# Kernel optimization log

Measured on AMD Instinct MI355X. Metric: run time of the kernel, lower is better.

## Reference

```python
import jax, jax.numpy as jnp
import numpy as np

BINS = 10
VMIN = 0.0
VMAX = 1.0
SIGMA = 150.0
DELTA = (VMAX - VMIN) / BINS


def setup_inputs() -> dict:
    key = jax.random.key(0)
    kx, ky = jax.random.split(key)
    x = jax.random.uniform(kx, (16, 3, 512, 512), dtype=jnp.float32)
    y = jax.random.uniform(ky, (16, 3, 512, 512), dtype=jnp.float32)
    return {"x": x, "y": y}


def _soft_hist(img):
    # img: [B, 3, H, W] -> soft histogram [B, 3, BINS]
    centers = VMIN + DELTA * (jnp.arange(BINS, dtype=img.dtype) + 0.5)
    d = img[..., None] - centers  # [B, 3, H, W, BINS]
    w = jax.nn.sigmoid(SIGMA * (d + DELTA / 2)) - jax.nn.sigmoid(SIGMA * (d - DELTA / 2))
    return w.sum(axis=(2, 3))  # sum over all pixels


def reference(x, y):
    B = x.shape[0]
    hx = _soft_hist(x)  # [B, 3, BINS]
    hy = _soft_hist(y)
    # L1Loss (mean over bins) per (batch, channel), summed over batch and channels
    running = jnp.abs(hx - hy).mean(axis=-1).sum()
    return (running / B) * 0.0001
```

## Files before the change

### kernel.cpp

```cpp
#include <hip/hip_runtime.h>


static constexpr int PLANES   = 48;
static constexpr int PLANE_PX = 512 * 512;
static constexpr int SPP      = 32;
static constexpr int THREADS  = 256;
static constexpr int CHUNK    = PLANE_PX / SPP;
static constexpr int NBLK     = 96 * SPP;
static constexpr float E15    = 3269017.3724721107f;

__global__ __launch_bounds__(THREADS, 8) void soft_hist_partial(
    const float* __restrict__ xin, const float* __restrict__ yin,
    unsigned* __restrict__ G )
{
  __shared__ unsigned hist[10 * THREADS];
  __shared__ unsigned red[10 * 16 * 3];
  const int t = threadIdx.x;
  #pragma unroll
  for (int s = 0; s < 10; ++s) hist[s * THREADS + t] = 0u;
  __syncthreads();

  const int blk   = blockIdx.x;
  const int plane = blk >> 5;
  const int sub   = blk & 31;
  const float* src = (plane < PLANES ? xin + (size_t)plane * PLANE_PX
                                     : yin + (size_t)(plane - PLANES) * PLANE_PX)
                   + (size_t)sub * CHUNK;
  const float4* src4 = (const float4*)src;
  unsigned* mycol = hist + t;

  constexpr int ITERS = CHUNK / (THREADS * 4);
  #pragma unroll
  for (int it = 0; it < ITERS; ++it) {
    float4 v4 = src4[it * THREADS + t];
    float vv[4] = {v4.x, v4.y, v4.z, v4.w};
    #pragma unroll
    for (int j = 0; j < 4; ++j) {
      float wv = vv[j] * 10.0f;
      float kf = fminf(floorf(wv), 9.0f);
      int   k  = (int)kf;
      float d  = wv - kf;
      float ex = __expf(d * -15.0f);
      float t1 = 1.0f + ex;
      float t2 = fmaf(E15, ex, 1.0f);
      float r  = __builtin_amdgcn_rcpf(t1 * t2);
      unsigned qa = (unsigned)fmaf(r * t2, 512.0f, 0.5f);
      unsigned qb = (unsigned)fmaf(r * t1, 64.0f, 0.5f);
      atomicAdd(&mycol[k << 8], (qa << 17) + (qb << 6) + 1u);
    }
  }
  __syncthreads();

  if (t < 160) {
    const int bin = t >> 4, grp = t & 15;
    const uint4* hp = (const uint4*)(hist + (bin << 8) + (grp << 4));
    unsigned sa = 0, sb = 0, sc = 0;
    #pragma unroll
    for (int q = 0; q < 4; ++q) {
      uint4 u4 = hp[q];
      unsigned uu[4] = {u4.x, u4.y, u4.z, u4.w};
      #pragma unroll
      for (int e = 0; e < 4; ++e) {
        unsigned u = uu[e];
        sa += u >> 17; sb += (u >> 6) & 0x7FFu; sc += u & 0x3Fu;
      }
    }
    const int base = (bin * 16 + grp) * 3;
    red[base] = sa; red[base + 1] = sb; red[base + 2] = sc;
  }
  __syncthreads();

  if (t < 30) {
    const int bin = t / 3, c = t - 3 * bin;
    unsigned s = 0;
    #pragma unroll
    for (int g = 0; g < 16; ++g) s += red[(bin * 16 + g) * 3 + c];
    G[blk * 32 + bin * 3 + c] = s;
  }
}

__global__ __launch_bounds__(1024) void soft_hist_loss(
    const unsigned* __restrict__ G, float* __restrict__ out)
{
  __shared__ unsigned T[96 * 30];
  __shared__ float wred[16];
  const int t = threadIdx.x;

  for (int item = t; item < 96 * 30; item += 1024) {
    const int plane = item / 30, comp = item - plane * 30;
    const unsigned* g = G + (size_t)plane * (32 * 32) + comp;
    unsigned s = 0;
    #pragma unroll
    for (int sub = 0; sub < 32; ++sub) s += g[sub * 32];
    T[item] = s;
  }
  __syncthreads();

  float val = 0.0f;
  if (t < 480) {
    const int pc = t / 10;
    const int i  = t - pc * 10;
    const unsigned* gx = T + pc * 30;
    const unsigned* gy = T + (pc + PLANES) * 30;
    float hx = (float)gx[3 * i] * (1.0f / 512.0f)
             - (float)gx[3 * i + 1] * (1.0f / 64.0f)
             + (i > 0 ? (float)gx[3 * (i - 1) + 1] * (1.0f / 64.0f) : 0.0f)
             + (i < 9 ? (float)gx[3 * (i + 1) + 2]
                      - (float)gx[3 * (i + 1)] * (1.0f / 512.0f) : 0.0f);
    float hy = (float)gy[3 * i] * (1.0f / 512.0f)
             - (float)gy[3 * i + 1] * (1.0f / 64.0f)
             + (i > 0 ? (float)gy[3 * (i - 1) + 1] * (1.0f / 64.0f) : 0.0f)
             + (i < 9 ? (float)gy[3 * (i + 1) + 2]
                      - (float)gy[3 * (i + 1)] * (1.0f / 512.0f) : 0.0f);
    val = fabsf(hx - hy);
  }
  #pragma unroll
  for (int off = 32; off >= 1; off >>= 1) val += __shfl_xor(val, off, 64);
  if ((t & 63) == 0) wred[t >> 6] = val;
  __syncthreads();
  if (t == 0) {
    float s = 0.0f;
    #pragma unroll
    for (int w = 0; w < 16; ++w) s += wred[w];
    out[0] = s * 6.25e-7f;
  }
}

extern "C" void kernel_launch(void* const* d_in, const int* in_sizes, int n_in,
                              void* d_out, int out_size, void* d_ws, size_t ws_size,
                              hipStream_t stream) {
  const float* x = (const float*)d_in[0];
  const float* y = (const float*)d_in[1];
  unsigned* G = (unsigned*)d_ws;
  soft_hist_partial<<<NBLK, THREADS, 0, stream>>>(x, y, G);
  soft_hist_loss<<<1, 1024, 0, stream>>>(G, (float*)d_out);
}
```

Before: 32.16 us.

## Prefetch loads two iterations ahead and reduce partials via global atomics

```diff
diff --git a/kernel.cpp b/kernel.cpp
--- a/kernel.cpp
+++ b/kernel.cpp
@@ -30,23 +30,28 @@
   unsigned* mycol = hist + t;
 
   constexpr int ITERS = CHUNK / (THREADS * 4);
+  float4 c0 = src4[t];
+  float4 c1 = src4[THREADS + t];
   #pragma unroll
   for (int it = 0; it < ITERS; ++it) {
-    float4 v4 = src4[it * THREADS + t];
-    float vv[4] = {v4.x, v4.y, v4.z, v4.w};
+    float4 cur = c0;
+    c0 = c1;
+    if (it + 2 < ITERS) c1 = src4[(it + 2) * THREADS + t];
+    float vv[4] = {cur.x, cur.y, cur.z, cur.w};
     #pragma unroll
     for (int j = 0; j < 4; ++j) {
       float wv = vv[j] * 10.0f;
-      float kf = fminf(floorf(wv), 9.0f);
-      int   k  = (int)kf;
-      float d  = wv - kf;
+      float d  = wv - floorf(wv);
+      int   k  = (int)wv;
+      k = k > 9 ? 9 : k;
       float ex = __expf(d * -15.0f);
       float t1 = 1.0f + ex;
       float t2 = fmaf(E15, ex, 1.0f);
       float r  = __builtin_amdgcn_rcpf(t1 * t2);
       unsigned qa = (unsigned)fmaf(r * t2, 512.0f, 0.5f);
       unsigned qb = (unsigned)fmaf(r * t1, 64.0f, 0.5f);
-      atomicAdd(&mycol[k << 8], (qa << 17) + (qb << 6) + 1u);
+      unsigned pk = (((qa << 11) + qb) << 6) + 1u;
+      atomicAdd(&mycol[k << 8], pk);
     }
   }
   __syncthreads();
@@ -75,33 +80,21 @@
     unsigned s = 0;
     #pragma unroll
     for (int g = 0; g < 16; ++g) s += red[(bin * 16 + g) * 3 + c];
-    G[blk * 32 + bin * 3 + c] = s;
+    atomicAdd(&G[plane * 30 + bin * 3 + c], s);
   }
 }
 
-__global__ __launch_bounds__(1024) void soft_hist_loss(
+__global__ __launch_bounds__(512) void soft_hist_loss(
     const unsigned* __restrict__ G, float* __restrict__ out)
 {
-  __shared__ unsigned T[96 * 30];
-  __shared__ float wred[16];
+  __shared__ float wred[8];
   const int t = threadIdx.x;
-
-  for (int item = t; item < 96 * 30; item += 1024) {
-    const int plane = item / 30, comp = item - plane * 30;
-    const unsigned* g = G + (size_t)plane * (32 * 32) + comp;
-    unsigned s = 0;
-    #pragma unroll
-    for (int sub = 0; sub < 32; ++sub) s += g[sub * 32];
-    T[item] = s;
-  }
-  __syncthreads();
-
   float val = 0.0f;
   if (t < 480) {
     const int pc = t / 10;
     const int i  = t - pc * 10;
-    const unsigned* gx = T + pc * 30;
-    const unsigned* gy = T + (pc + PLANES) * 30;
+    const unsigned* gx = G + pc * 30;
+    const unsigned* gy = G + (pc + PLANES) * 30;
     float hx = (float)gx[3 * i] * (1.0f / 512.0f)
              - (float)gx[3 * i + 1] * (1.0f / 64.0f)
              + (i > 0 ? (float)gx[3 * (i - 1) + 1] * (1.0f / 64.0f) : 0.0f)
@@ -121,7 +114,7 @@
   if (t == 0) {
     float s = 0.0f;
     #pragma unroll
-    for (int w = 0; w < 16; ++w) s += wred[w];
+    for (int w = 0; w < 8; ++w) s += wred[w];
     out[0] = s * 6.25e-7f;
   }
 }
@@ -132,6 +125,7 @@
   const float* x = (const float*)d_in[0];
   const float* y = (const float*)d_in[1];
   unsigned* G = (unsigned*)d_ws;
+  hipMemsetAsync(d_ws, 0, 96 * 30 * sizeof(unsigned), stream);
   soft_hist_partial<<<NBLK, THREADS, 0, stream>>>(x, y, G);
-  soft_hist_loss<<<1, 1024, 0, stream>>>(G, (float*)d_out);
+  soft_hist_loss<<<1, 512, 0, stream>>>(G, (float*)d_out);
 }
```

Result: no change. 31.91 us (-0.8%).
